# Optimization experiments

Hardware: AMD Instinct MI355X
Metric: run time of the kernel (lower is better)

## Reference

```python
import jax, jax.numpy as jnp
import numpy as np

DIM_SED = 256
DIM_DOA = 256
DIM_ATTN = 256
NUM_HEADS = 8
HEAD_DIM = DIM_ATTN // NUM_HEADS
SCALE = HEAD_DIM ** -0.5
B, N_SED, N_DOA = 2, 2048, 2048


def setup_inputs() -> dict:
    key = jax.random.key(0)
    ks = jax.random.split(key, 8)
    s = lambda fan_in: 1.0 / np.sqrt(fan_in)
    return {
        "x_sed": jax.random.normal(ks[0], (B, N_SED, DIM_SED), jnp.float32),
        "x_doa": jax.random.normal(ks[1], (B, N_DOA, DIM_DOA), jnp.float32),
        # nn.Linear stores weight as [out, in]; we keep [in, out] for x @ W
        "W_sed_in": jax.random.uniform(ks[2], (DIM_SED, 2 * DIM_ATTN), jnp.float32, -s(DIM_SED), s(DIM_SED)),
        "W_doa_in": jax.random.uniform(ks[3], (DIM_DOA, 2 * DIM_ATTN), jnp.float32, -s(DIM_DOA), s(DIM_DOA)),
        "W_sed_out": jax.random.uniform(ks[4], (DIM_ATTN, DIM_SED), jnp.float32, -s(DIM_ATTN), s(DIM_ATTN)),
        "b_sed_out": jax.random.uniform(ks[5], (DIM_SED,), jnp.float32, -s(DIM_ATTN), s(DIM_ATTN)),
        "W_doa_out": jax.random.uniform(ks[6], (DIM_ATTN, DIM_DOA), jnp.float32, -s(DIM_ATTN), s(DIM_ATTN)),
        "b_doa_out": jax.random.uniform(ks[7], (DIM_DOA,), jnp.float32, -s(DIM_ATTN), s(DIM_ATTN)),
    }


def _split_heads(rv, B, N):
    # rv: [B, N, 2*DIM_ATTN] -> r, v each [B, H, N, hd]
    rv = rv.reshape(B, N, 2, NUM_HEADS, HEAD_DIM).transpose(2, 0, 3, 1, 4)
    return rv[0], rv[1]


def reference(x_sed, x_doa, W_sed_in, W_doa_in, W_sed_out, b_sed_out, W_doa_out, b_doa_out):
    B_, Ns, _ = x_sed.shape
    _, Nd, _ = x_doa.shape
    r_sed, v_sed = _split_heads(x_sed @ W_sed_in, B_, Ns)  # [B,H,Ns,hd]
    r_doa, v_doa = _split_heads(x_doa @ W_doa_in, B_, Nd)  # [B,H,Nd,hd]

    # Shared score matrix, softmaxed in both directions (dropout = identity, eval mode)
    attn = jnp.einsum('bhsd,bhtd->bhst', r_sed, r_doa) * SCALE  # [B,H,Ns,Nd]
    attn_sed2doa = jax.nn.softmax(attn, axis=-1)               # row-wise
    attn_doa2sed = jax.nn.softmax(attn, axis=-2)               # col-wise (softmax of attn^T over last dim)

    x_sed_fused = jnp.einsum('bhst,bhtd->bhsd', attn_sed2doa, v_doa)
    x_sed_fused = x_sed_fused.transpose(0, 2, 1, 3).reshape(B_, Ns, DIM_ATTN)
    x_sed_fused = x_sed_fused @ W_sed_out + b_sed_out

    x_doa_fused = jnp.einsum('bhst,bhsd->bhtd', attn_doa2sed, v_sed)
    x_doa_fused = x_doa_fused.transpose(0, 2, 1, 3).reshape(B_, Nd, DIM_ATTN)
    x_doa_fused = x_doa_fused @ W_doa_out + b_doa_out
    return (x_sed_fused, x_doa_fused)
```

## Files before the change

### kernel.cpp

```cpp
#include <hip/hip_runtime.h>
#include <hip/hip_bf16.h>

typedef short short8 __attribute__((ext_vector_type(8)));
typedef float f32x4 __attribute__((ext_vector_type(4)));
typedef float f32x16 __attribute__((ext_vector_type(16)));
typedef unsigned int uint4v __attribute__((ext_vector_type(4)));
typedef unsigned short ushort_t;

__device__ inline ushort_t f2bf(float f) {
    union { float f; unsigned u; } x; x.f = f;
    unsigned r = x.u + 0x7fffu + ((x.u >> 16) & 1u);
    return (ushort_t)(r >> 16);
}
__device__ inline ushort_t f2bf_u(float x) {
    union { __hip_bfloat16 h; ushort_t u; } cv;
    cv.h = __float2bfloat16(x);
    return cv.u;
}
__device__ inline float bf2f(ushort_t u) {
    union { unsigned u; float f; } cv; cv.u = ((unsigned)u) << 16; return cv.f;
}

#define GLD_LDS16(src, dst)                                                  \
    __builtin_amdgcn_global_load_lds(                                        \
        (const __attribute__((address_space(1))) void*)(src),                \
        (__attribute__((address_space(3))) void*)(dst), 16, 0, 0)

#define RSQ 0.5050100f

__global__ __launch_bounds__(256) void prep_w_kernel(const float* __restrict__ w0,
                                                     const float* __restrict__ w1,
                                                     const float* __restrict__ w2,
                                                     const float* __restrict__ w3,
                                                     ushort_t* __restrict__ t0,
                                                     ushort_t* __restrict__ t1,
                                                     ushort_t* __restrict__ t2,
                                                     ushort_t* __restrict__ t3) {
    int z = blockIdx.y;
    const float* W; ushort_t* T; int J;
    if (z == 0)      { W = w0; T = t0; J = 512; }
    else if (z == 1) { W = w1; T = t1; J = 512; }
    else if (z == 2) { W = w2; T = t2; J = 256; }
    else             { W = w3; T = t3; J = 256; }
    int idx = blockIdx.x * 256 + threadIdx.x;
    if (idx >= J * 256) return;
    int k = idx & 255, j = idx >> 8;
    T[idx] = f2bf(W[k * J + j]);
}

__global__ __launch_bounds__(256) void gemm_in_kernel(
    const float* __restrict__ A0, const float* __restrict__ A1,
    const ushort_t* __restrict__ B0, const ushort_t* __restrict__ B1,
    ushort_t* __restrict__ R0, ushort_t* __restrict__ R1,
    ushort_t* __restrict__ V0, ushort_t* __restrict__ V1) {
    const float* A = blockIdx.z ? A1 : A0;
    const ushort_t* Bt = blockIdx.z ? B1 : B0;
    ushort_t* R = blockIdx.z ? R1 : R0;
    ushort_t* Vt = blockIdx.z ? V1 : V0;
    constexpr int K = 256;
    const int w = threadIdx.x >> 6, lane = threadIdx.x & 63;
    const int l16 = lane & 15, g = lane >> 4;
    const int m0 = blockIdx.x * 64 + w * 16;
    const int cb = blockIdx.y * 64;

    f32x4 acc[4] = {};
    const float* Ap = A + (size_t)(m0 + l16) * K + 8 * g;
    const ushort_t* Bp = Bt + (size_t)(cb + l16) * K + 8 * g;

    #pragma unroll
    for (int ks = 0; ks < K; ks += 32) {
        float4 af0 = *reinterpret_cast<const float4*>(Ap + ks);
        float4 af1 = *reinterpret_cast<const float4*>(Ap + ks + 4);
        short8 a;
        a[0] = (short)f2bf_u(af0.x); a[1] = (short)f2bf_u(af0.y);
        a[2] = (short)f2bf_u(af0.z); a[3] = (short)f2bf_u(af0.w);
        a[4] = (short)f2bf_u(af1.x); a[5] = (short)f2bf_u(af1.y);
        a[6] = (short)f2bf_u(af1.z); a[7] = (short)f2bf_u(af1.w);
        #pragma unroll
        for (int c = 0; c < 4; ++c) {
            short8 b = *reinterpret_cast<const short8*>(Bp + (size_t)c * 16 * K + ks);
            acc[c] = __builtin_amdgcn_mfma_f32_16x16x32_bf16(a, b, acc[c], 0, 0, 0);
        }
    }

    if (blockIdx.y < 4) {
        #pragma unroll
        for (int c = 0; c < 4; ++c) {
            int col = cb + c * 16 + l16;
            int h = col >> 5, d = col & 31;
            #pragma unroll
            for (int r = 0; r < 4; ++r) {
                int row = m0 + 4 * g + r;
                int bb = row >> 11, n = row & 2047;
                size_t base = (size_t)(bb * 8 + h) * 65536;
                int unit = ((n >> 5) * 4 + (d >> 4) * 2 + ((d >> 3) & 1)) * 32 + (n & 31);
                R[base + (size_t)unit * 8 + (d & 7)] = f2bf_u(acc[c][r] * RSQ);
            }
        }
    } else {
        #pragma unroll
        for (int c = 0; c < 4; ++c) {
            int colp = cb - 256 + c * 16 + l16;
            int h = colp >> 5, d = colp & 31;
            int row = m0 + 4 * g;
            int bb = row >> 11, n = row & 2047;
            size_t base = (size_t)(bb * 8 + h) * 65536;
            int nl = n & 31;
            int vh = nl >> 4, r4 = nl & 15;
            int hi2 = (r4 >> 2) & 1;
            int e0 = (r4 & 3) + 4 * (r4 >> 3);
            int unit = ((n >> 5) * 4 + vh * 2 + hi2) * 32 + d;
            ushort4 s;
            s.x = f2bf_u(acc[c][0]); s.y = f2bf_u(acc[c][1]);
            s.z = f2bf_u(acc[c][2]); s.w = f2bf_u(acc[c][3]);
            *reinterpret_cast<ushort4*>(Vt + base + (size_t)unit * 8 + e0) = s;
        }
    }
}

__global__ __launch_bounds__(512, 4) void attn_kernel(
    const ushort_t* __restrict__ rU_sed, const ushort_t* __restrict__ rU_doa,
    const ushort_t* __restrict__ vU_sed, const ushort_t* __restrict__ vU_doa,
    ushort_t* __restrict__ part,
    float* __restrict__ lpart) {
    __shared__ __align__(16) ushort_t smem[8192];

    const int bid = blockIdx.x;
    const int xcd = bid & 7, i = bid >> 3;
    const int stream = xcd * 4 + (i & 3);
    const int rest = i >> 2;
    const int qblk = rest & 7, kvh = rest >> 3;
    const int dir = stream >> 4, bh = stream & 15;

    const ushort_t* rQ = dir ? rU_doa : rU_sed;
    const ushort_t* rK = dir ? rU_sed : rU_doa;
    const ushort_t* vV = dir ? vU_sed : vU_doa;

    const int tid = threadIdx.x;
    const int w = tid >> 6, lane = tid & 63;
    const int l31 = lane & 31, hi = lane >> 5;
    const size_t sB = (size_t)bh * 65536;
    const int qbase = qblk * 256 + w * 32;

    const short8 qf0 = *reinterpret_cast<const short8*>(rQ + sB + (size_t)qbase * 32 + lane * 8);
    const short8 qf1 = *reinterpret_cast<const short8*>(rQ + sB + (size_t)qbase * 32 + 512 + lane * 8);

    const ushort_t* Kbase = rK + sB + (size_t)kvh * 32768;
    const ushort_t* Vbase = vV + sB + (size_t)kvh * 32768;
    const ushort_t* srcK = Kbase + tid * 8;
    const int dstK = w * 512;

    f32x16 acc = {};
    f32x4 lv = {};

    int buf = 0;
    GLD_LDS16(srcK, &smem[dstK]);
    __syncthreads();

    for (int t = 0; t < 8; ++t) {
        if (t < 7) GLD_LDS16(srcK + (size_t)(t + 1) * 4096, &smem[(buf ^ 1) * 4096 + dstK]);
        const ushort_t* KB = &smem[buf * 4096];
        const ushort_t* Vt = Vbase + (size_t)t * 4096;
        #pragma unroll
        for (int s = 0; s < 4; ++s) {
            short8 kf0 = *reinterpret_cast<const short8*>(KB + s * 1024 + lane * 8);
            short8 kf1 = *reinterpret_cast<const short8*>(KB + s * 1024 + 512 + lane * 8);
            short8 vf0 = *reinterpret_cast<const short8*>(Vt + s * 1024 + lane * 8);
            short8 vf1 = *reinterpret_cast<const short8*>(Vt + s * 1024 + 512 + lane * 8);

            f32x16 z16 = {};
            f32x16 st = __builtin_amdgcn_mfma_f32_32x32x16_bf16(kf0, qf0, z16, 0, 0, 0);
            st = __builtin_amdgcn_mfma_f32_32x32x16_bf16(kf1, qf1, st, 0, 0, 0);

            float p[16];
            #pragma unroll
            for (int j = 0; j < 16; ++j) {
                p[j] = __builtin_amdgcn_exp2f(st[j]);
            }
            #pragma unroll
            for (int j = 0; j < 16; ++j) lv[j & 3] += p[j];

            unsigned pk[8];
            #pragma unroll
            for (int j = 0; j < 8; ++j) {
                asm("v_cvt_pk_bf16_f32 %0, %1, %2" : "=v"(pk[j]) : "v"(p[2 * j]), "v"(p[2 * j + 1]));
            }
            union { uint4v u; short8 s; } c1, c2;
            c1.u = uint4v{pk[0], pk[1], pk[2], pk[3]};
            c2.u = uint4v{pk[4], pk[5], pk[6], pk[7]};

            acc = __builtin_amdgcn_mfma_f32_32x32x16_bf16(vf0, c1.s, acc, 0, 0, 0);
            acc = __builtin_amdgcn_mfma_f32_32x32x16_bf16(vf1, c2.s, acc, 0, 0, 0);
        }
        __syncthreads();
        buf ^= 1;
    }

    float l = (lv[0] + lv[1]) + (lv[2] + lv[3]);
    l += __shfl_xor(l, 32);
    const int q = qbase + l31;
    const size_t prow = ((size_t)stream * 2 + kvh) * 2048 + q;
    if (lane < 32) lpart[prow] = l;
    ushort_t* pa = part + prow * 32;
    #pragma unroll
    for (int r = 0; r < 16; ++r) {
        int d = (r & 3) + 8 * (r >> 2) + 4 * hi;
        pa[d] = f2bf(acc[r]);
    }
}

__global__ __launch_bounds__(256) void gemm_out_kernel(
    const ushort_t* __restrict__ part, const float* __restrict__ lpart,
    const ushort_t* __restrict__ b0, const ushort_t* __restrict__ b1,
    float* __restrict__ c0, float* __restrict__ c1,
    const float* __restrict__ bias0, const float* __restrict__ bias1) {
    const int z = blockIdx.z;
    const ushort_t* Bt = z ? b1 : b0;
    float* C = z ? c1 : c0;
    const float* bias = z ? bias1 : bias0;
    constexpr int K = 256, N = 256;
    const int w = threadIdx.x >> 6, lane = threadIdx.x & 63;
    const int l16 = lane & 15, g = lane >> 4;
    const int m0 = blockIdx.x * 64 + w * 16;
    const int cb = blockIdx.y * 64;

    const int row = m0 + l16;
    const int bb = row >> 11, q = row & 2047;

    f32x4 acc[4] = {};
    const ushort_t* Bp = Bt + (size_t)(cb + l16) * K + 8 * g;
    #pragma unroll
    for (int it = 0; it < 8; ++it) {
        const int strm = z * 16 + bb * 8 + it;
        const size_t pr0 = ((size_t)strm * 2) * 2048 + q;
        float l0 = lpart[pr0], l1 = lpart[pr0 + 2048];
        float inv = 1.0f / (l0 + l1);
        const ushort_t* p0 = part + pr0 * 32 + 8 * g;
        const ushort_t* p1 = p0 + (size_t)2048 * 32;
        short8 pa = *reinterpret_cast<const short8*>(p0);
        short8 pb = *reinterpret_cast<const short8*>(p1);
        short8 a;
        #pragma unroll
        for (int e = 0; e < 8; ++e) {
            a[e] = (short)f2bf_u((bf2f((ushort_t)pa[e]) + bf2f((ushort_t)pb[e])) * inv);
        }
        #pragma unroll
        for (int c = 0; c < 4; ++c) {
            short8 b = *reinterpret_cast<const short8*>(Bp + (size_t)c * 16 * K + it * 32);
            acc[c] = __builtin_amdgcn_mfma_f32_16x16x32_bf16(a, b, acc[c], 0, 0, 0);
        }
    }
    #pragma unroll
    for (int c = 0; c < 4; ++c) {
        int col = cb + c * 16 + l16;
        #pragma unroll
        for (int r = 0; r < 4; ++r) {
            int orow = m0 + 4 * g + r;
            C[(size_t)orow * N + col] = acc[c][r] + bias[col];
        }
    }
}

extern "C" void kernel_launch(void* const* d_in, const int* in_sizes, int n_in,
                              void* d_out, int out_size, void* d_ws, size_t ws_size,
                              hipStream_t stream) {
    const float* x_sed     = (const float*)d_in[0];
    const float* x_doa     = (const float*)d_in[1];
    const float* W_sed_in  = (const float*)d_in[2];
    const float* W_doa_in  = (const float*)d_in[3];
    const float* W_sed_out = (const float*)d_in[4];
    const float* b_sed_out = (const float*)d_in[5];
    const float* W_doa_out = (const float*)d_in[6];
    const float* b_doa_out = (const float*)d_in[7];
    float* out = (float*)d_out;

    ushort_t* ws = (ushort_t*)d_ws;
    ushort_t* wt_si  = ws;
    ushort_t* wt_di  = wt_si  + 131072;
    ushort_t* wt_so  = wt_di  + 131072;
    ushort_t* wt_do  = wt_so  + 65536;
    ushort_t* rU_sed = wt_do  + 65536;
    ushort_t* rU_doa = rU_sed + 1048576;
    ushort_t* vU_sed = rU_doa + 1048576;
    ushort_t* vU_doa = vU_sed + 1048576;
    ushort_t* part   = vU_doa + 1048576;
    float*    lpart  = (float*)(part + 4194304);

    prep_w_kernel<<<dim3(512, 4), 256, 0, stream>>>(W_sed_in, W_doa_in, W_sed_out, W_doa_out,
                                                    wt_si, wt_di, wt_so, wt_do);
    gemm_in_kernel<<<dim3(64, 8, 2), 256, 0, stream>>>(x_sed, x_doa, wt_si, wt_di,
                                                       rU_sed, rU_doa, vU_sed, vU_doa);
    attn_kernel<<<dim3(512), 512, 0, stream>>>(rU_sed, rU_doa, vU_sed, vU_doa, part, lpart);
    gemm_out_kernel<<<dim3(64, 4, 2), 256, 0, stream>>>(part, lpart, wt_so, wt_do,
                                                        out, out + 1048576, b_sed_out, b_doa_out);
}
```

Before: 70.25 us.

## Tile weight transpose via LDS, widen GEMM column tiles, stage V through LDS

The weight-prep kernel now transposes 64x64 tiles through shared memory, so both the global reads and the bf16 writes are coalesced and vectorized instead of strided scalar accesses. The input and output projection GEMMs each compute 128 columns per block instead of 64, so every converted A fragment is reused across twice as many MFMAs, at the cost of half as many blocks and more accumulator registers. The attention kernel now double-buffers V tiles into LDS with async global-to-LDS loads alongside K, instead of reading V fragments straight from global memory. This doubles LDS use per block, which may limit occupancy.

```diff
diff --git a/kernel.cpp b/kernel.cpp
--- a/kernel.cpp
+++ b/kernel.cpp
@@ -36,16 +36,37 @@
                                                      ushort_t* __restrict__ t1,
                                                      ushort_t* __restrict__ t2,
                                                      ushort_t* __restrict__ t3) {
+    __shared__ float tile[64][65];
     int z = blockIdx.y;
     const float* W; ushort_t* T; int J;
     if (z == 0)      { W = w0; T = t0; J = 512; }
     else if (z == 1) { W = w1; T = t1; J = 512; }
     else if (z == 2) { W = w2; T = t2; J = 256; }
     else             { W = w3; T = t3; J = 256; }
-    int idx = blockIdx.x * 256 + threadIdx.x;
-    if (idx >= J * 256) return;
-    int k = idx & 255, j = idx >> 8;
-    T[idx] = f2bf(W[k * J + j]);
+    int ntj = J >> 6;
+    int nt = ntj * 4;
+    int tix = blockIdx.x;
+    if (tix >= nt) return;
+    int tj = tix % ntj, tk = tix / ntj;
+    int j0 = tj * 64, k0 = tk * 64;
+    int tid = threadIdx.x;
+
+    int jj = (tid & 15) * 4, kk0 = tid >> 4;
+    #pragma unroll
+    for (int kk = kk0; kk < 64; kk += 16) {
+        float4 v = *reinterpret_cast<const float4*>(&W[(size_t)(k0 + kk) * J + j0 + jj]);
+        tile[kk][jj] = v.x; tile[kk][jj + 1] = v.y;
+        tile[kk][jj + 2] = v.z; tile[kk][jj + 3] = v.w;
+    }
+    __syncthreads();
+    int kk4 = (tid & 15) * 4, jj0 = tid >> 4;
+    #pragma unroll
+    for (int j2 = jj0; j2 < 64; j2 += 16) {
+        ushort4 o;
+        o.x = f2bf(tile[kk4][j2]);     o.y = f2bf(tile[kk4 + 1][j2]);
+        o.z = f2bf(tile[kk4 + 2][j2]); o.w = f2bf(tile[kk4 + 3][j2]);
+        *reinterpret_cast<ushort4*>(&T[(size_t)(j0 + j2) * 256 + k0 + kk4]) = o;
+    }
 }
 
 __global__ __launch_bounds__(256) void gemm_in_kernel(
@@ -61,9 +82,9 @@
     const int w = threadIdx.x >> 6, lane = threadIdx.x & 63;
     const int l16 = lane & 15, g = lane >> 4;
     const int m0 = blockIdx.x * 64 + w * 16;
-    const int cb = blockIdx.y * 64;
-
-    f32x4 acc[4] = {};
+    const int cb = blockIdx.y * 128;
+
+    f32x4 acc[8] = {};
     const float* Ap = A + (size_t)(m0 + l16) * K + 8 * g;
     const ushort_t* Bp = Bt + (size_t)(cb + l16) * K + 8 * g;
 
@@ -77,15 +98,15 @@
         a[4] = (short)f2bf_u(af1.x); a[5] = (short)f2bf_u(af1.y);
         a[6] = (short)f2bf_u(af1.z); a[7] = (short)f2bf_u(af1.w);
         #pragma unroll
-        for (int c = 0; c < 4; ++c) {
+        for (int c = 0; c < 8; ++c) {
             short8 b = *reinterpret_cast<const short8*>(Bp + (size_t)c * 16 * K + ks);
             acc[c] = __builtin_amdgcn_mfma_f32_16x16x32_bf16(a, b, acc[c], 0, 0, 0);
         }
     }
 
-    if (blockIdx.y < 4) {
-        #pragma unroll
-        for (int c = 0; c < 4; ++c) {
+    if (blockIdx.y < 2) {
+        #pragma unroll
+        for (int c = 0; c < 8; ++c) {
             int col = cb + c * 16 + l16;
             int h = col >> 5, d = col & 31;
             #pragma unroll
@@ -99,7 +120,7 @@
         }
     } else {
         #pragma unroll
-        for (int c = 0; c < 4; ++c) {
+        for (int c = 0; c < 8; ++c) {
             int colp = cb - 256 + c * 16 + l16;
             int h = colp >> 5, d = colp & 31;
             int row = m0 + 4 * g;
@@ -123,7 +144,7 @@
     const ushort_t* __restrict__ vU_sed, const ushort_t* __restrict__ vU_doa,
     ushort_t* __restrict__ part,
     float* __restrict__ lpart) {
-    __shared__ __align__(16) ushort_t smem[8192];
+    __shared__ __align__(16) ushort_t smem[16384];
 
     const int bid = blockIdx.x;
     const int xcd = bid & 7, i = bid >> 3;
@@ -148,25 +169,32 @@
     const ushort_t* Kbase = rK + sB + (size_t)kvh * 32768;
     const ushort_t* Vbase = vV + sB + (size_t)kvh * 32768;
     const ushort_t* srcK = Kbase + tid * 8;
+    const ushort_t* srcV = Vbase + tid * 8;
     const int dstK = w * 512;
+    const int dstV = 4096 + w * 512;
 
     f32x16 acc = {};
     f32x4 lv = {};
 
+    auto stage = [&](int t, int bufsel) {
+        GLD_LDS16(srcK + (size_t)t * 4096, &smem[bufsel * 8192 + dstK]);
+        GLD_LDS16(srcV + (size_t)t * 4096, &smem[bufsel * 8192 + dstV]);
+    };
+
     int buf = 0;
-    GLD_LDS16(srcK, &smem[dstK]);
+    stage(0, 0);
     __syncthreads();
 
     for (int t = 0; t < 8; ++t) {
-        if (t < 7) GLD_LDS16(srcK + (size_t)(t + 1) * 4096, &smem[(buf ^ 1) * 4096 + dstK]);
-        const ushort_t* KB = &smem[buf * 4096];
-        const ushort_t* Vt = Vbase + (size_t)t * 4096;
+        if (t < 7) stage(t + 1, buf ^ 1);
+        const ushort_t* KB = &smem[buf * 8192];
+        const ushort_t* VB = &smem[buf * 8192 + 4096];
         #pragma unroll
         for (int s = 0; s < 4; ++s) {
             short8 kf0 = *reinterpret_cast<const short8*>(KB + s * 1024 + lane * 8);
             short8 kf1 = *reinterpret_cast<const short8*>(KB + s * 1024 + 512 + lane * 8);
-            short8 vf0 = *reinterpret_cast<const short8*>(Vt + s * 1024 + lane * 8);
-            short8 vf1 = *reinterpret_cast<const short8*>(Vt + s * 1024 + 512 + lane * 8);
+            short8 vf0 = *reinterpret_cast<const short8*>(VB + s * 1024 + lane * 8);
+            short8 vf1 = *reinterpret_cast<const short8*>(VB + s * 1024 + 512 + lane * 8);
 
             f32x16 z16 = {};
             f32x16 st = __builtin_amdgcn_mfma_f32_32x32x16_bf16(kf0, qf0, z16, 0, 0, 0);
@@ -222,12 +250,12 @@
     const int w = threadIdx.x >> 6, lane = threadIdx.x & 63;
     const int l16 = lane & 15, g = lane >> 4;
     const int m0 = blockIdx.x * 64 + w * 16;
-    const int cb = blockIdx.y * 64;
+    const int cb = blockIdx.y * 128;
 
     const int row = m0 + l16;
     const int bb = row >> 11, q = row & 2047;
 
-    f32x4 acc[4] = {};
+    f32x4 acc[8] = {};
     const ushort_t* Bp = Bt + (size_t)(cb + l16) * K + 8 * g;
     #pragma unroll
     for (int it = 0; it < 8; ++it) {
@@ -245,13 +273,13 @@
             a[e] = (short)f2bf_u((bf2f((ushort_t)pa[e]) + bf2f((ushort_t)pb[e])) * inv);
         }
         #pragma unroll
-        for (int c = 0; c < 4; ++c) {
+        for (int c = 0; c < 8; ++c) {
             short8 b = *reinterpret_cast<const short8*>(Bp + (size_t)c * 16 * K + it * 32);
             acc[c] = __builtin_amdgcn_mfma_f32_16x16x32_bf16(a, b, acc[c], 0, 0, 0);
         }
     }
     #pragma unroll
-    for (int c = 0; c < 4; ++c) {
+    for (int c = 0; c < 8; ++c) {
         int col = cb + c * 16 + l16;
         #pragma unroll
         for (int r = 0; r < 4; ++r) {
@@ -286,11 +314,11 @@
     ushort_t* part   = vU_doa + 1048576;
     float*    lpart  = (float*)(part + 4194304);
 
-    prep_w_kernel<<<dim3(512, 4), 256, 0, stream>>>(W_sed_in, W_doa_in, W_sed_out, W_doa_out,
-                                                    wt_si, wt_di, wt_so, wt_do);
-    gemm_in_kernel<<<dim3(64, 8, 2), 256, 0, stream>>>(x_sed, x_doa, wt_si, wt_di,
+    prep_w_kernel<<<dim3(32, 4), 256, 0, stream>>>(W_sed_in, W_doa_in, W_sed_out, W_doa_out,
+                                                   wt_si, wt_di, wt_so, wt_do);
+    gemm_in_kernel<<<dim3(64, 4, 2), 256, 0, stream>>>(x_sed, x_doa, wt_si, wt_di,
                                                        rU_sed, rU_doa, vU_sed, vU_doa);
     attn_kernel<<<dim3(512), 512, 0, stream>>>(rU_sed, rU_doa, vU_sed, vU_doa, part, lpart);
-    gemm_out_kernel<<<dim3(64, 4, 2), 256, 0, stream>>>(part, lpart, wt_so, wt_do,
+    gemm_out_kernel<<<dim3(64, 2, 2), 256, 0, stream>>>(part, lpart, wt_so, wt_do,
                                                         out, out + 1048576, b_sed_out, b_doa_out);
 }
```

New measurement: 67.52 us, median of 2. 1.04x faster.
